# Kernel optimization log

Hardware: AMD Instinct MI355X
Metric: run time of the kernel (lower is better)

Reference implementation:

```python
import jax, jax.numpy as jnp
import numpy as np

LEN = 4          # self.lenth: 4x4 window grid -> max seq len 16
HEADS = 16
SHIFT = LEN // 2 # cyclic shift of lenth//2 in generate_mask


def _build_mask(n):
    # generate_mask(h=heads//2, w=2, p=LEN, shift=SHIFT), type != 'W'
    h, w, p = HEADS // 2, 2, LEN
    s = p - SHIFT
    m = np.zeros((h, w, p, p, p, p), dtype=bool)
    m[-1, :, :s, :, s:, :] = True
    m[-1, :, s:, :, :s, :] = True
    m[:, -1, :, :s, :, s:] = True
    m[:, -1, :, s:, :, :s] = True
    # 'w1 w2 p1 p2 p3 p4 -> 1 (w1 w2) (p1 p2) (p3 p4)' (contiguous merge)
    m = m.reshape(1, h * w, p * p, p * p)
    return jnp.asarray(m[:, :, :n, :n])


def _rel_indices(n):
    cord = np.array([[i, j] for i in range(LEN) for j in range(LEN)])  # (16,2)
    rel = cord[:n, None, :] - cord[None, :n, :] + LEN - 1              # (n,n,2)
    return rel[..., 0], rel[..., 1]


def setup_inputs() -> dict:
    key = jax.random.key(0)
    ks = jax.random.split(key, 6)
    b, n, dim = 4096, 16, 512
    inner = HEADS * 64  # heads * dim_head = 1024
    return {
        "x": jax.random.normal(ks[0], (b, n, dim), dtype=jnp.float32),
        "w_qkv": jax.random.normal(ks[1], (3 * inner, dim), dtype=jnp.float32) * 0.02,
        "b_qkv": jax.random.normal(ks[2], (3 * inner,), dtype=jnp.float32) * 0.02,
        "w_proj": jax.random.normal(ks[3], (dim, inner), dtype=jnp.float32) * 0.02,
        "b_proj": jax.random.normal(ks[4], (dim,), dtype=jnp.float32) * 0.02,
        "rel_pos": jax.random.normal(ks[5], (HEADS, 2 * LEN - 1, 2 * LEN - 1), dtype=jnp.float32) * 0.02,
    }


def reference(x, w_qkv, b_qkv, w_proj, b_proj, rel_pos):
    b, n, _ = x.shape
    h = HEADS
    # type != 'W' -> cyclic shift along tokens
    x = jnp.roll(x, -(n // 2), axis=1)
    qkv = x @ w_qkv.T + b_qkv                       # (b, n, 3*inner)
    q, k, v = jnp.split(qkv, 3, axis=-1)
    split = lambda t: t.reshape(b, n, h, -1).transpose(0, 2, 1, 3)  # b h n d
    q, k, v = split(q), split(k), split(v)
    scale = q.shape[-1] ** -0.5
    dots = jnp.einsum('bhid,bhjd->bhij', q, k) * scale
    r0, r1 = _rel_indices(n)
    dots = dots + rel_pos[:, r0, r1][None]          # (1, h, n, n) rel-pos bias
    mask = _build_mask(n)                           # (1, h, n, n) bool
    dots = jnp.where(mask, -jnp.inf, dots)
    attn = jax.nn.softmax(dots, axis=-1)
    out = jnp.einsum('bhij,bhjd->bhid', attn, v)
    out = out.transpose(0, 2, 1, 3).reshape(b, n, -1)  # (b, n, inner)
    return out @ w_proj.T + b_proj
```

## Files before the change

### kernel.cpp

```cpp
#include <hip/hip_runtime.h>
#include <stdint.h>


typedef __attribute__((ext_vector_type(8))) short frag8;
typedef __attribute__((ext_vector_type(4))) float frag4f;

__device__ __forceinline__ uint16_t f2bf(float f) {
  union { float f; uint32_t i; } x; x.f = f;
  uint32_t r = x.i + 0x7fffu + ((x.i >> 16) & 1u);
  return (uint16_t)(r >> 16);
}

#define SCHED0() __builtin_amdgcn_sched_barrier(0)


__global__ __launch_bounds__(256)
void k_cvt3(const float* __restrict__ sx, const float* __restrict__ sq,
            const float* __restrict__ sp, uint16_t* __restrict__ dx,
            uint16_t* __restrict__ dq, uint16_t* __restrict__ dp, int ok)
{
  if (!ok) return;
  const int n0 = 33554432 / 4, n1 = 1572864 / 4, n2 = 524288 / 4;
  int i = blockIdx.x * 256 + threadIdx.x;
  const int stride = gridDim.x * 256;
  for (; i < n0 + n1 + n2; i += stride) {
    const float* s; uint16_t* d; int k;
    if (i < n0)           { s = sx; d = dx; k = i; }
    else if (i < n0 + n1) { s = sq; d = dq; k = i - n0; }
    else                  { s = sp; d = dp; k = i - n0 - n1; }
    float4 v = ((const float4*)s)[k];
    ushort4 o;
    o.x = f2bf(v.x); o.y = f2bf(v.y); o.z = f2bf(v.z); o.w = f2bf(v.w);
    ((ushort4*)d)[k] = o;
  }
}


struct SmemEpi  { uint16_t q[128][68]; uint16_t k[128][68];
                  uint16_t vT[64][132]; };
union Smem1 { uint8_t g[2][20480]; SmemEpi e; };

__global__ __launch_bounds__(256, 3)
void k_qkv_attn(const uint16_t* __restrict__ xb, const uint16_t* __restrict__ wqkvb,
                const float* __restrict__ b_qkv, const float* __restrict__ rel_pos,
                uint16_t* __restrict__ attn16, int ws_ok)
{
  __shared__ Smem1 sm;
  const int bid  = blockIdx.x;
  const int lgc  = ((bid & 7) << 10) | (bid >> 3);
  const int h    = lgc & 15;
  const int mt   = lgc >> 4;
  const int t    = threadIdx.x;
  const int lane = t & 63;
  const int wv   = t >> 6;
  const int l15  = lane & 15;
  const int quad = lane >> 4;
  const int wr   = wv & 1;
  const int wc   = wv >> 1;

  if (!ws_ok) {
    #pragma unroll
    for (int i = 0; i < 32; ++i) {
      const int local = t + 256 * i;
      const int row = local >> 6, col = local & 63;
      attn16[(mt * 128 + row) * 1024 + h * 64 + col] = 0;
    }
    return;
  }

  const int slot_g = (lane & 3) ^ ((lane >> 3) & 3);
  const uint16_t* sp[5];
  int ldsoff[5];
  #pragma unroll
  for (int o = 0; o < 5; ++o) {
    const int c = wv * 5 + o;
    const int rloc = c * 16 + (lane >> 2);
    if (c < 8) {
      const int g = mt * 128 + rloc;
      const int srow = (g & ~15) | ((g + 8) & 15);
      sp[o] = xb + srow * 512 + slot_g * 8;
    } else {
      const int cb = rloc - 128;
      const int gc = (cb < 64) ? (h * 64 + cb)
                   : (cb < 128) ? (1024 + h * 64 + (cb - 64))
                                : (2048 + h * 64 + (cb - 128));
      sp[o] = wqkvb + gc * 512 + slot_g * 8;
    }
    ldsoff[o] = c * 1024;
  }

  frag4f acc[4][6];
  #pragma unroll
  for (int a = 0; a < 4; ++a)
    #pragma unroll
    for (int b = 0; b < 6; ++b) acc[a][b] = (frag4f)0.0f;

  auto STAGE = [&](int buf, int kk) {
    #pragma unroll
    for (int o = 0; o < 5; ++o)
      __builtin_amdgcn_global_load_lds(
          (const __attribute__((address_space(1))) void*)(sp[o] + kk * 32),
          (__attribute__((address_space(3))) void*)(sm.g[buf] + ldsoff[o]),
          16, 0, 0);
  };

  STAGE(0, 0);

  const int xq = quad ^ ((l15 >> 1) & 3);
  for (int kk = 0; kk < 16; ++kk) {
    const int cur = kk & 1;
    if (kk < 15) {
      STAGE(cur ^ 1, kk + 1);
      SCHED0();
      asm volatile("s_waitcnt vmcnt(5)" ::: "memory");
    } else {
      SCHED0();
      asm volatile("s_waitcnt vmcnt(0)" ::: "memory");
    }
    SCHED0();
    __builtin_amdgcn_s_barrier();
    SCHED0();

    const uint8_t* base = sm.g[cur];
    frag8 af[4], bf[6];
    #pragma unroll
    for (int rt = 0; rt < 4; ++rt)
      af[rt] = *(const frag8*)(base + (wr * 64 + rt * 16 + l15) * 64 + xq * 16);
    #pragma unroll
    for (int ct = 0; ct < 6; ++ct)
      bf[ct] = *(const frag8*)(base + 8192 + ((wc * 6 + ct) * 16 + l15) * 64 + xq * 16);
    #pragma unroll
    for (int rt = 0; rt < 4; ++rt)
      #pragma unroll
      for (int ct = 0; ct < 6; ++ct)
        acc[rt][ct] = __builtin_amdgcn_mfma_f32_16x16x32_bf16(af[rt], bf[ct], acc[rt][ct], 0, 0, 0);

    SCHED0();
    asm volatile("s_waitcnt lgkmcnt(0)" ::: "memory");
    SCHED0();
    __builtin_amdgcn_s_barrier();
    SCHED0();
  }

  #pragma unroll
  for (int ct = 0; ct < 6; ++ct) {
    const int C = (wc * 6 + ct) * 16 + l15;
    const int gc = (C < 64) ? (h * 64 + C)
                 : (C < 128) ? (1024 + h * 64 + (C - 64))
                             : (2048 + h * 64 + (C - 128));
    const float bias = b_qkv[gc];
    #pragma unroll
    for (int rt = 0; rt < 4; ++rt) {
      #pragma unroll
      for (int r = 0; r < 4; ++r) {
        const int row = wr * 64 + rt * 16 + quad * 4 + r;
        const uint16_t val = f2bf(acc[rt][ct][r] + bias);
        if (C < 64)       sm.e.q[row][C] = val;
        else if (C < 128) sm.e.k[row][C - 64] = val;
        else              sm.e.vT[C - 128][row] = val;
      }
    }
  }
  __syncthreads();

  const float scl = 0.125f;
  frag8 qa0[2], qa1[2], kb0[2], kb1[2];
  frag4f s2[2];
  #pragma unroll
  for (int bbi = 0; bbi < 2; ++bbi) {
    const int bb = wv * 2 + bbi;
    qa0[bbi] = *(const frag8*)&sm.e.q[bb * 16 + l15][quad * 8];
    qa1[bbi] = *(const frag8*)&sm.e.q[bb * 16 + l15][32 + quad * 8];
    kb0[bbi] = *(const frag8*)&sm.e.k[bb * 16 + l15][quad * 8];
    kb1[bbi] = *(const frag8*)&sm.e.k[bb * 16 + l15][32 + quad * 8];
  }
  #pragma unroll
  for (int bbi = 0; bbi < 2; ++bbi) {
    frag4f s = (frag4f)0.0f;
    s = __builtin_amdgcn_mfma_f32_16x16x32_bf16(kb0[bbi], qa0[bbi], s, 0, 0, 0);
    s = __builtin_amdgcn_mfma_f32_16x16x32_bf16(kb1[bbi], qa1[bbi], s, 0, 0, 0);
    s2[bbi] = s;
  }
  __syncthreads();

  uint16_t (*pp)[16][20] = (uint16_t (*)[16][20])sm.e.q;
  #pragma unroll
  for (int bbi = 0; bbi < 2; ++bbi) {
    const int bb = wv * 2 + bbi;
    const int i = l15;
    float v[4];
    #pragma unroll
    for (int r = 0; r < 4; ++r) {
      const int j = quad * 4 + r;
      const int r0 = (i >> 2) - (j >> 2) + 3;
      const int r1 = (i & 3) - (j & 3) + 3;
      const float bias = rel_pos[h * 49 + r0 * 7 + r1];
      const bool msk = ((h >= 14) && (((i >> 2) < 2) != ((j >> 2) < 2))) ||
                       ((h & 1)  && (((i & 3) < 2) != ((j & 3) < 2)));
      v[r] = msk ? -1e30f : (s2[bbi][r] * scl + bias);
    }
    float m = fmaxf(fmaxf(v[0], v[1]), fmaxf(v[2], v[3]));
    m = fmaxf(m, __shfl_xor(m, 16));
    m = fmaxf(m, __shfl_xor(m, 32));
    float e0 = __expf(v[0] - m), e1 = __expf(v[1] - m);
    float e2 = __expf(v[2] - m), e3 = __expf(v[3] - m);
    float su = (e0 + e1) + (e2 + e3);
    su += __shfl_xor(su, 16);
    su += __shfl_xor(su, 32);
    const float rs = 1.0f / su;
    ushort4 pk;
    pk.x = f2bf(e0 * rs); pk.y = f2bf(e1 * rs);
    pk.z = f2bf(e2 * rs); pk.w = f2bf(e3 * rs);
    *(ushort4*)&pp[bb][i][quad * 4] = pk;
  }
  __syncthreads();

  #pragma unroll
  for (int bbi = 0; bbi < 2; ++bbi) {
    const int bb = wv * 2 + bbi;
    frag8 pb;
    if (quad < 2) pb = *(const frag8*)&pp[bb][l15][quad * 8];
    else          pb = (frag8)0;
    #pragma unroll
    for (int dt = 0; dt < 4; ++dt) {
      frag8 av = *(const frag8*)&sm.e.vT[dt * 16 + l15][bb * 16 + (quad & 1) * 8];
      frag4f o = (frag4f)0.0f;
      o = __builtin_amdgcn_mfma_f32_16x16x32_bf16(av, pb, o, 0, 0, 0);
      ushort4 ok4;
      ok4.x = f2bf(o[0]); ok4.y = f2bf(o[1]);
      ok4.z = f2bf(o[2]); ok4.w = f2bf(o[3]);
      const int grow = mt * 128 + bb * 16 + l15;
      *(ushort4*)&attn16[grow * 1024 + h * 64 + dt * 16 + quad * 4] = ok4;
    }
  }
}


__global__ __launch_bounds__(512, 4)
void k_proj(const uint16_t* __restrict__ attn16, const uint16_t* __restrict__ wprojb,
            const float* __restrict__ b_proj, float* __restrict__ out, int ws_ok)
{
  __shared__ uint8_t smraw[2 * 36864];
  const int mt   = blockIdx.x;
  const int t    = threadIdx.x;
  const int lane = t & 63;
  const int wv   = t >> 6;
  const int l15  = lane & 15;
  const int quad = lane >> 4;

  if (!ws_ok) {
    for (int i = t; i < 64 * 512; i += 512) {
      const int row = i >> 9, col = i & 511;
      out[(mt * 64 + row) * 512 + col] = b_proj[col];
    }
    return;
  }

  const int cnt = (wv < 4) ? 5 : 4;
  const int c0  = (wv < 4) ? wv * 5 : 20 + (wv - 4) * 4;
  const int slot_g = (lane & 3) ^ ((lane >> 3) & 3);

  const uint16_t* gp[5];
  int lds_off[5];
  #pragma unroll
  for (int o = 0; o < 5; ++o) {
    int c = c0 + o;
    if (c > 35) c = 35;
    const int rloc = c * 16 + (lane >> 2);
    if (c < 4) {
      gp[o] = attn16 + (size_t)(mt * 64 + rloc) * 1024 + slot_g * 8;
    } else {
      gp[o] = wprojb + (size_t)(rloc - 64) * 1024 + slot_g * 8;
    }
    lds_off[o] = (c0 + o) * 1024;
  }

  frag4f acc[4][4];
  #pragma unroll
  for (int a = 0; a < 4; ++a)
    #pragma unroll
    for (int b = 0; b < 4; ++b) acc[a][b] = (frag4f)0.0f;

  auto STAGE = [&](int buf, int kk) {
    #pragma unroll
    for (int o = 0; o < 5; ++o)
      if (o < cnt)
        __builtin_amdgcn_global_load_lds(
            (const __attribute__((address_space(1))) void*)(gp[o] + kk * 32),
            (__attribute__((address_space(3))) void*)(smraw + buf * 36864 + lds_off[o]),
            16, 0, 0);
  };

  STAGE(0, 0);
  __syncthreads();

  const int xq = quad ^ ((l15 >> 1) & 3);
  for (int kk = 0; kk < 32; ++kk) {
    const int cur = kk & 1;
    if (kk < 31) STAGE(cur ^ 1, kk + 1);

    const uint16_t* As = (const uint16_t*)(smraw + cur * 36864);
    const uint16_t* Bs = (const uint16_t*)(smraw + cur * 36864 + 4096);
    frag8 af[4];
    #pragma unroll
    for (int rt = 0; rt < 4; ++rt)
      af[rt] = *(const frag8*)(As + (rt * 16 + l15) * 32 + xq * 8);
    #pragma unroll
    for (int ct = 0; ct < 4; ++ct) {
      frag8 bfr = *(const frag8*)(Bs + (wv * 64 + ct * 16 + l15) * 32 + xq * 8);
      #pragma unroll
      for (int rt = 0; rt < 4; ++rt)
        acc[rt][ct] = __builtin_amdgcn_mfma_f32_16x16x32_bf16(af[rt], bfr, acc[rt][ct], 0, 0, 0);
    }
    __syncthreads();
  }

  #pragma unroll
  for (int ct = 0; ct < 4; ++ct) {
    const int gcol = wv * 64 + ct * 16 + l15;
    const float bias = b_proj[gcol];
    #pragma unroll
    for (int rt = 0; rt < 4; ++rt) {
      #pragma unroll
      for (int r = 0; r < 4; ++r) {
        const int grow = mt * 64 + rt * 16 + quad * 4 + r;
        out[grow * 512 + gcol] = acc[rt][ct][r] + bias;
      }
    }
  }
}


extern "C" void kernel_launch(void* const* d_in, const int* in_sizes, int n_in,
                              void* d_out, int out_size, void* d_ws, size_t ws_size,
                              hipStream_t stream) {
  const float* x      = (const float*)d_in[0];
  const float* w_qkv  = (const float*)d_in[1];
  const float* b_qkv  = (const float*)d_in[2];
  const float* w_proj = (const float*)d_in[3];
  const float* b_proj = (const float*)d_in[4];
  const float* rel    = (const float*)d_in[5];

  uint16_t* xb     = (uint16_t*)d_ws;
  uint16_t* wqkvb  = xb + 33554432;
  uint16_t* wprojb = wqkvb + 1572864;
  const size_t ws_need = (size_t)(33554432 + 1572864 + 524288) * 2;
  const int ws_ok = (ws_size >= ws_need) ? 1 : 0;

  uint16_t* attn16 = (uint16_t*)d_out;
  float*    out    = (float*)d_out;

  k_cvt3<<<dim3(2048), dim3(256), 0, stream>>>(x, w_qkv, w_proj, xb, wqkvb, wprojb, ws_ok);
  k_qkv_attn<<<dim3(512 * 16), dim3(256), 0, stream>>>(xb, wqkvb, b_qkv, rel, attn16, ws_ok);
  k_proj    <<<dim3(1024),     dim3(512), 0, stream>>>(attn16, wprojb, b_proj, out, ws_ok);
}
```

Before: 604.6 us.

## Retile projection GEMM to 128-row blocks with triple-buffered async loads

The projection kernel now uses 1024-thread blocks, each covering 128 output rows, with a 2x8 wave grid and three LDS stages. Loads run two iterations ahead, and explicit vmcnt waits with raw barriers replace __syncthreads, so global-to-LDS traffic overlaps the MFMA work and each projection-weight tile is reused across more rows. The fp32-to-bf16 conversion kernel now gives each block a fixed contiguous chunk instead of a grid-stride loop with per-element branching. The QKV MFMA loop is wrapped in s_setprio to raise wave priority during matrix math. The trade-off is that the larger LDS footprint leaves room for only one projection block per CU, which lowers occupancy.

```diff
diff --git a/kernel.cpp b/kernel.cpp
--- a/kernel.cpp
+++ b/kernel.cpp
@@ -20,18 +20,16 @@
             uint16_t* __restrict__ dq, uint16_t* __restrict__ dp, int ok)
 {
   if (!ok) return;
-  const int n0 = 33554432 / 4, n1 = 1572864 / 4, n2 = 524288 / 4;
-  int i = blockIdx.x * 256 + threadIdx.x;
-  const int stride = gridDim.x * 256;
-  for (; i < n0 + n1 + n2; i += stride) {
-    const float* s; uint16_t* d; int k;
-    if (i < n0)           { s = sx; d = dx; k = i; }
-    else if (i < n0 + n1) { s = sq; d = dq; k = i - n0; }
-    else                  { s = sp; d = dp; k = i - n0 - n1; }
-    float4 v = ((const float4*)s)[k];
+  const int b = blockIdx.x;
+  const float* s; uint16_t* d; int base, n;
+  if (b < 2048)      { s = sx; d = dx; base = b * 4096;          n = 4096; }
+  else if (b < 2240) { s = sq; d = dq; base = (b - 2048) * 2048; n = 2048; }
+  else               { s = sp; d = dp; base = (b - 2240) * 2048; n = 2048; }
+  for (int i = threadIdx.x; i < n; i += 256) {
+    float4 v = ((const float4*)s)[base + i];
     ushort4 o;
     o.x = f2bf(v.x); o.y = f2bf(v.y); o.z = f2bf(v.z); o.w = f2bf(v.w);
-    ((ushort4*)d)[k] = o;
+    ((ushort4*)d)[base + i] = o;
   }
 }
 
@@ -129,11 +127,13 @@
     #pragma unroll
     for (int ct = 0; ct < 6; ++ct)
       bf[ct] = *(const frag8*)(base + 8192 + ((wc * 6 + ct) * 16 + l15) * 64 + xq * 16);
+    __builtin_amdgcn_s_setprio(1);
     #pragma unroll
     for (int rt = 0; rt < 4; ++rt)
       #pragma unroll
       for (int ct = 0; ct < 6; ++ct)
         acc[rt][ct] = __builtin_amdgcn_mfma_f32_16x16x32_bf16(af[rt], bf[ct], acc[rt][ct], 0, 0, 0);
+    __builtin_amdgcn_s_setprio(0);
 
     SCHED0();
     asm volatile("s_waitcnt lgkmcnt(0)" ::: "memory");
@@ -236,41 +236,43 @@
 }
 
 
-__global__ __launch_bounds__(512, 4)
+__global__ __launch_bounds__(1024, 4)
 void k_proj(const uint16_t* __restrict__ attn16, const uint16_t* __restrict__ wprojb,
             const float* __restrict__ b_proj, float* __restrict__ out, int ws_ok)
 {
-  __shared__ uint8_t smraw[2 * 36864];
+  __shared__ uint8_t smraw[3 * 40960];
   const int mt   = blockIdx.x;
   const int t    = threadIdx.x;
   const int lane = t & 63;
   const int wv   = t >> 6;
   const int l15  = lane & 15;
   const int quad = lane >> 4;
+  const int wr2  = wv & 1;
+  const int wc8  = wv >> 1;
 
   if (!ws_ok) {
-    for (int i = t; i < 64 * 512; i += 512) {
+    for (int i = t; i < 128 * 512; i += 1024) {
       const int row = i >> 9, col = i & 511;
-      out[(mt * 64 + row) * 512 + col] = b_proj[col];
+      out[(mt * 128 + row) * 512 + col] = b_proj[col];
     }
     return;
   }
 
-  const int cnt = (wv < 4) ? 5 : 4;
-  const int c0  = (wv < 4) ? wv * 5 : 20 + (wv - 4) * 4;
+  const int cnt = (wv < 8) ? 3 : 2;
+  const int c0  = (wv < 8) ? wv * 3 : 24 + (wv - 8) * 2;
   const int slot_g = (lane & 3) ^ ((lane >> 3) & 3);
 
-  const uint16_t* gp[5];
-  int lds_off[5];
-  #pragma unroll
-  for (int o = 0; o < 5; ++o) {
+  const uint16_t* gp[3];
+  int lds_off[3];
+  #pragma unroll
+  for (int o = 0; o < 3; ++o) {
     int c = c0 + o;
-    if (c > 35) c = 35;
+    if (c > 39) c = 39;
     const int rloc = c * 16 + (lane >> 2);
-    if (c < 4) {
-      gp[o] = attn16 + (size_t)(mt * 64 + rloc) * 1024 + slot_g * 8;
+    if (c < 8) {
+      gp[o] = attn16 + (size_t)(mt * 128 + rloc) * 1024 + slot_g * 8;
     } else {
-      gp[o] = wprojb + (size_t)(rloc - 64) * 1024 + slot_g * 8;
+      gp[o] = wprojb + (size_t)(rloc - 128) * 1024 + slot_g * 8;
     }
     lds_off[o] = (c0 + o) * 1024;
   }
@@ -283,47 +285,69 @@
 
   auto STAGE = [&](int buf, int kk) {
     #pragma unroll
-    for (int o = 0; o < 5; ++o)
+    for (int o = 0; o < 3; ++o)
       if (o < cnt)
         __builtin_amdgcn_global_load_lds(
             (const __attribute__((address_space(1))) void*)(gp[o] + kk * 32),
-            (__attribute__((address_space(3))) void*)(smraw + buf * 36864 + lds_off[o]),
+            (__attribute__((address_space(3))) void*)(smraw + buf * 40960 + lds_off[o]),
             16, 0, 0);
   };
 
   STAGE(0, 0);
-  __syncthreads();
+  STAGE(1, 1);
 
   const int xq = quad ^ ((l15 >> 1) & 3);
+  int cur = 0;
   for (int kk = 0; kk < 32; ++kk) {
-    const int cur = kk & 1;
-    if (kk < 31) STAGE(cur ^ 1, kk + 1);
-
-    const uint16_t* As = (const uint16_t*)(smraw + cur * 36864);
-    const uint16_t* Bs = (const uint16_t*)(smraw + cur * 36864 + 4096);
+    if (kk < 30) {
+      int nb = cur + 2; if (nb >= 3) nb -= 3;
+      STAGE(nb, kk + 2);
+      SCHED0();
+      if (wv < 8) asm volatile("s_waitcnt vmcnt(6)" ::: "memory");
+      else        asm volatile("s_waitcnt vmcnt(4)" ::: "memory");
+    } else if (kk == 30) {
+      SCHED0();
+      if (wv < 8) asm volatile("s_waitcnt vmcnt(3)" ::: "memory");
+      else        asm volatile("s_waitcnt vmcnt(2)" ::: "memory");
+    } else {
+      SCHED0();
+      asm volatile("s_waitcnt vmcnt(0)" ::: "memory");
+    }
+    SCHED0();
+    __builtin_amdgcn_s_barrier();
+    SCHED0();
+
+    const uint16_t* As = (const uint16_t*)(smraw + cur * 40960);
+    const uint16_t* Bs = (const uint16_t*)(smraw + cur * 40960 + 8192);
     frag8 af[4];
     #pragma unroll
     for (int rt = 0; rt < 4; ++rt)
-      af[rt] = *(const frag8*)(As + (rt * 16 + l15) * 32 + xq * 8);
+      af[rt] = *(const frag8*)(As + (wr2 * 64 + rt * 16 + l15) * 32 + xq * 8);
     #pragma unroll
     for (int ct = 0; ct < 4; ++ct) {
-      frag8 bfr = *(const frag8*)(Bs + (wv * 64 + ct * 16 + l15) * 32 + xq * 8);
+      frag8 bfr = *(const frag8*)(Bs + (wc8 * 64 + ct * 16 + l15) * 32 + xq * 8);
       #pragma unroll
       for (int rt = 0; rt < 4; ++rt)
         acc[rt][ct] = __builtin_amdgcn_mfma_f32_16x16x32_bf16(af[rt], bfr, acc[rt][ct], 0, 0, 0);
     }
-    __syncthreads();
+
+    SCHED0();
+    asm volatile("s_waitcnt lgkmcnt(0)" ::: "memory");
+    SCHED0();
+    __builtin_amdgcn_s_barrier();
+    SCHED0();
+    ++cur; if (cur >= 3) cur -= 3;
   }
 
   #pragma unroll
   for (int ct = 0; ct < 4; ++ct) {
-    const int gcol = wv * 64 + ct * 16 + l15;
+    const int gcol = wc8 * 64 + ct * 16 + l15;
     const float bias = b_proj[gcol];
     #pragma unroll
     for (int rt = 0; rt < 4; ++rt) {
       #pragma unroll
       for (int r = 0; r < 4; ++r) {
-        const int grow = mt * 64 + rt * 16 + quad * 4 + r;
+        const int grow = mt * 128 + wr2 * 64 + rt * 16 + quad * 4 + r;
         out[grow * 512 + gcol] = acc[rt][ct][r] + bias;
       }
     }
@@ -350,7 +374,7 @@
   uint16_t* attn16 = (uint16_t*)d_out;
   float*    out    = (float*)d_out;
 
-  k_cvt3<<<dim3(2048), dim3(256), 0, stream>>>(x, w_qkv, w_proj, xb, wqkvb, wprojb, ws_ok);
+  k_cvt3<<<dim3(2304), dim3(256), 0, stream>>>(x, w_qkv, w_proj, xb, wqkvb, wprojb, ws_ok);
   k_qkv_attn<<<dim3(512 * 16), dim3(256), 0, stream>>>(xb, wqkvb, b_qkv, rel, attn16, ws_ok);
-  k_proj    <<<dim3(1024),     dim3(512), 0, stream>>>(attn16, wprojb, b_proj, out, ws_ok);
-}
+  k_proj    <<<dim3(512),      dim3(1024), 0, stream>>>(attn16, wprojb, b_proj, out, ws_ok);
+}
```

Result: no change. 598.6 us (-1.0%).
